# Kernel tuning notes

Hardware: AMD Instinct MI355X
Metric: run time of the kernel (lower is better)

## Reference

```python
import jax, jax.numpy as jnp
import numpy as np

V = 50257       # vocab size (leaves of Huffman tree)
N_DEC = V - 1   # internal decision nodes
D = 1024        # input_size
N_EX = 8192     # number of examples (tokens)
MAX_LEN = 24    # max Huffman path depth


def setup_inputs() -> dict:
    key = jax.random.key(0)
    k_x, k_w, k_t, k_p, k_c, k_l = jax.random.split(key, 6)
    x = jax.random.normal(k_x, (N_EX, D), dtype=jnp.float32)
    W = jax.random.normal(k_w, (N_DEC, D), dtype=jnp.float32) * 0.02
    t = jax.random.randint(k_t, (N_EX,), 0, V, dtype=jnp.int32)
    # padded per-leaf tree paths: decision-node indices and +/-1 branch codes
    paths = jax.random.randint(k_p, (V, MAX_LEN), 0, N_DEC, dtype=jnp.int32)
    codes = jnp.where(jax.random.bernoulli(k_c, 0.5, (V, MAX_LEN)), 1.0, -1.0).astype(jnp.float32)
    lens = jax.random.randint(k_l, (V,), 1, MAX_LEN + 1, dtype=jnp.int32)
    return {"x": x, "W": W, "t": t, "paths": paths, "codes": codes, "lens": lens}


def reference(x, W, t, paths, codes, lens):
    # Per-example tree path: gather the decision nodes / codes for each target leaf.
    node_idx = paths[t]            # [N_EX, MAX_LEN] int32
    code = codes[t]                # [N_EX, MAX_LEN] +/-1
    mask = (jnp.arange(MAX_LEN)[None, :] < lens[t][:, None]).astype(x.dtype)  # [N_EX, MAX_LEN]
    # Irregular gather of W rows along each path, then per-step dot products.
    Wp = W[node_idx]               # [N_EX, MAX_LEN, D]
    wxy = code * jnp.einsum('nd,nld->nl', x, Wp)   # [N_EX, MAX_LEN]
    # Per-decision binary log-loss: log(1 + exp(-wxy)), masked to true path length.
    ls = jax.nn.softplus(-wxy) * mask
    return ls.sum()
```

## Files before the change

### kernel.cpp

```cpp
#include <hip/hip_runtime.h>
#include <math.h>

#define HS_D       1024
#define HS_MAXLEN  24

__global__ __launch_bounds__(256) void hsm_ex_kernel(
    const float* __restrict__ x,
    const float* __restrict__ W,
    const int*   __restrict__ t,
    const int*   __restrict__ paths,
    const float* __restrict__ codes,
    const int*   __restrict__ lens,
    float*       __restrict__ ws,
    int n_ex)
{
    const int tid  = threadIdx.x;
    const int lane = tid & 63;
    const int n = __builtin_amdgcn_readfirstlane(blockIdx.x * 4 + (tid >> 6));
    if (n >= n_ex) return;

    const int leaf = __builtin_amdgcn_readfirstlane(t[n]);
    const int L    = __builtin_amdgcn_readfirstlane(lens[leaf]);

    const float4* x4 = (const float4*)(x + (size_t)n * HS_D);
    float4 xf[4];
#pragma unroll
    for (int j = 0; j < 4; ++j) xf[j] = x4[j * 64 + lane];

    const int*   prow = paths + leaf * HS_MAXLEN;
    const float* crow = codes + leaf * HS_MAXLEN;

    float vsum = 0.0f;

    for (int l0 = 0; l0 < L; l0 += 2) {
        const int  l1 = l0 + 1;
        const bool v1 = (l1 < L);

        const int   node0 = __builtin_amdgcn_readfirstlane(prow[l0]);
        const float c0    = crow[l0];
        const int   node1 = __builtin_amdgcn_readfirstlane(v1 ? prow[l1] : node0);
        const float c1    = v1 ? crow[l1] : 1.0f;

        const float4* w0 = (const float4*)(W + (size_t)node0 * HS_D);
        const float4* w1 = (const float4*)(W + (size_t)node1 * HS_D);

        float4 wf0[4], wf1[4];
#pragma unroll
        for (int j = 0; j < 4; ++j) wf0[j] = w0[j * 64 + lane];
#pragma unroll
        for (int j = 0; j < 4; ++j) wf1[j] = w1[j * 64 + lane];

        float d0 = 0.0f, d1 = 0.0f;
#pragma unroll
        for (int j = 0; j < 4; ++j) {
            d0 += xf[j].x * wf0[j].x + xf[j].y * wf0[j].y
                + xf[j].z * wf0[j].z + xf[j].w * wf0[j].w;
            d1 += xf[j].x * wf1[j].x + xf[j].y * wf1[j].y
                + xf[j].z * wf1[j].z + xf[j].w * wf1[j].w;
        }

#pragma unroll
        for (int off = 32; off > 0; off >>= 1) {
            d0 += __shfl_xor(d0, off);
            d1 += __shfl_xor(d1, off);
        }

        const float z0 = -c0 * d0;
        float v = fmaxf(z0, 0.0f) + log1pf(expf(-fabsf(z0)));
        if (v1) {
            const float z1 = -c1 * d1;
            v += fmaxf(z1, 0.0f) + log1pf(expf(-fabsf(z1)));
        }
        vsum += v;
    }

    if (lane == 0) ws[n] = vsum;
}

__global__ __launch_bounds__(256) void hsm_finish_kernel(
    const float* __restrict__ ws, float* __restrict__ out, int n_ex)
{
    __shared__ float part[4];
    const int tid = threadIdx.x;

    float s = 0.0f;
    const int n4 = n_ex >> 2;
    const float4* w4 = (const float4*)ws;
    for (int k = tid; k < n4; k += 256) {
        const float4 v = w4[k];
        s += v.x + v.y + v.z + v.w;
    }
    if (tid < (n_ex & 3)) s += ws[(n_ex & ~3) + tid];

#pragma unroll
    for (int off = 32; off > 0; off >>= 1)
        s += __shfl_xor(s, off);

    if ((tid & 63) == 0) part[tid >> 6] = s;
    __syncthreads();
    if (tid == 0) out[0] = part[0] + part[1] + part[2] + part[3];
}

extern "C" void kernel_launch(void* const* d_in, const int* in_sizes, int n_in,
                              void* d_out, int out_size, void* d_ws, size_t ws_size,
                              hipStream_t stream) {
    const float* x     = (const float*)d_in[0];
    const float* W     = (const float*)d_in[1];
    const int*   t     = (const int*)  d_in[2];
    const int*   paths = (const int*)  d_in[3];
    const float* codes = (const float*)d_in[4];
    const int*   lens  = (const int*)  d_in[5];
    float* out = (float*)d_out;
    float* ws  = (float*)d_ws;

    const int n_ex = in_sizes[2];

    const int n_blocks = (n_ex + 3) / 4;
    hsm_ex_kernel<<<n_blocks, 256, 0, stream>>>(x, W, t, paths, codes, lens,
                                                ws, n_ex);
    hsm_finish_kernel<<<1, 256, 0, stream>>>(ws, out, n_ex);
}
```

Before: 335.0 us.

## Flatten tree-path pairs into a compacted work list, one wavefront per pair

A new build kernel expands each example's Huffman path into packed 64-bit (node0, node1, example, code-sign) pair entries, compacted through an atomic counter. The pair kernel then gives each wavefront one pair, which removes the serial per-example loop over variable path lengths and exposes more independent memory-latency parallelism. Per-pair losses are accumulated with float atomics into 512 buckets that the finish kernel sums. In exchange it adds a workspace memset, an extra launch, reloads x once per pair (from cache), and launches waves for the maximum pair count, many of which exit immediately.

```diff
diff --git a/kernel.cpp b/kernel.cpp
--- a/kernel.cpp
+++ b/kernel.cpp
@@ -3,99 +3,126 @@
 
 #define HS_D       1024
 #define HS_MAXLEN  24
+#define HS_MAXPAIR 12
+#define HS_NBUCKET 512
 
-__global__ __launch_bounds__(256) void hsm_ex_kernel(
-    const float* __restrict__ x,
-    const float* __restrict__ W,
+#define WS_BUCKET_OFF 64
+#define WS_WL_OFF     4096
+
+
+__global__ __launch_bounds__(64) void hsm_build_kernel(
     const int*   __restrict__ t,
     const int*   __restrict__ paths,
     const float* __restrict__ codes,
     const int*   __restrict__ lens,
-    float*       __restrict__ ws,
+    int*                 counter,
+    unsigned long long* __restrict__ wl,
     int n_ex)
+{
+    const int n = blockIdx.x * 64 + threadIdx.x;
+    if (n >= n_ex) return;
+
+    const int leaf  = t[n];
+    const int L     = lens[leaf];
+    const int npair = (L + 1) >> 1;
+
+    const int4*   p4 = (const int4*)(paths + leaf * HS_MAXLEN);
+    const float4* c4 = (const float4*)(codes + leaf * HS_MAXLEN);
+    int   pa[HS_MAXLEN];
+    float ca[HS_MAXLEN];
+#pragma unroll
+    for (int j = 0; j < HS_MAXLEN / 4; ++j) {
+        const int4   pv = p4[j];
+        const float4 cv = c4[j];
+        pa[4*j+0] = pv.x; pa[4*j+1] = pv.y; pa[4*j+2] = pv.z; pa[4*j+3] = pv.w;
+        ca[4*j+0] = cv.x; ca[4*j+1] = cv.y; ca[4*j+2] = cv.z; ca[4*j+3] = cv.w;
+    }
+
+    const int base = atomicAdd(counter, npair);
+
+#pragma unroll
+    for (int p = 0; p < HS_MAXPAIR; ++p) {
+        if (p < npair) {
+            const int  l0 = 2 * p, l1 = l0 + 1;
+            const bool v1 = (l1 < L);
+            const int  node0 = pa[l0];
+            const int  node1 = v1 ? pa[l1] : node0;
+            const unsigned c0s = (ca[l0] < 0.0f) ? 1u : 0u;
+            const unsigned c1s = (v1 && ca[l1] < 0.0f) ? 1u : 0u;
+            const unsigned lo  = (unsigned)node0 | ((unsigned)node1 << 16);
+            const unsigned hi  = (unsigned)n | (c0s << 24) | (c1s << 25)
+                               | (v1 ? (1u << 26) : 0u) | (1u << 28);
+            wl[base + p] = ((unsigned long long)hi << 32) | lo;
+        }
+    }
+}
+
+__global__ __launch_bounds__(256) void hsm_pair_kernel(
+    const float* __restrict__ x,
+    const float* __restrict__ W,
+    const unsigned long long* __restrict__ wl,
+    float*       __restrict__ buckets)
 {
     const int tid  = threadIdx.x;
     const int lane = tid & 63;
-    const int n = __builtin_amdgcn_readfirstlane(blockIdx.x * 4 + (tid >> 6));
-    if (n >= n_ex) return;
+    const int gw   = blockIdx.x * 4 + (tid >> 6);
 
-    const int leaf = __builtin_amdgcn_readfirstlane(t[n]);
-    const int L    = __builtin_amdgcn_readfirstlane(lens[leaf]);
+    const unsigned long long e = wl[gw];
+    const unsigned hi = (unsigned)(e >> 32);
+    if (!(hi & (1u << 28))) return;
 
-    const float4* x4 = (const float4*)(x + (size_t)n * HS_D);
-    float4 xf[4];
+    const unsigned lo = (unsigned)e;
+    const int n     = __builtin_amdgcn_readfirstlane((int)(hi & 0xFFFFFF));
+    const int node0 = __builtin_amdgcn_readfirstlane((int)(lo & 0xFFFFu));
+    const int node1 = __builtin_amdgcn_readfirstlane((int)(lo >> 16));
+    const float c0  = (hi & (1u << 24)) ? -1.0f : 1.0f;
+    const float c1  = (hi & (1u << 25)) ? -1.0f : 1.0f;
+    const float v1f = (hi & (1u << 26)) ? 1.0f : 0.0f;
+
+    const float4* x4 = (const float4*)(x + (size_t)n     * HS_D);
+    const float4* w0 = (const float4*)(W + (size_t)node0 * HS_D);
+    const float4* w1 = (const float4*)(W + (size_t)node1 * HS_D);
+
+    float4 xf[4], wf0[4], wf1[4];
 #pragma unroll
-    for (int j = 0; j < 4; ++j) xf[j] = x4[j * 64 + lane];
+    for (int j = 0; j < 4; ++j) xf[j]  = x4[j * 64 + lane];
+#pragma unroll
+    for (int j = 0; j < 4; ++j) wf0[j] = w0[j * 64 + lane];
+#pragma unroll
+    for (int j = 0; j < 4; ++j) wf1[j] = w1[j * 64 + lane];
 
-    const int*   prow = paths + leaf * HS_MAXLEN;
-    const float* crow = codes + leaf * HS_MAXLEN;
-
-    float vsum = 0.0f;
-
-    for (int l0 = 0; l0 < L; l0 += 2) {
-        const int  l1 = l0 + 1;
-        const bool v1 = (l1 < L);
-
-        const int   node0 = __builtin_amdgcn_readfirstlane(prow[l0]);
-        const float c0    = crow[l0];
-        const int   node1 = __builtin_amdgcn_readfirstlane(v1 ? prow[l1] : node0);
-        const float c1    = v1 ? crow[l1] : 1.0f;
-
-        const float4* w0 = (const float4*)(W + (size_t)node0 * HS_D);
-        const float4* w1 = (const float4*)(W + (size_t)node1 * HS_D);
-
-        float4 wf0[4], wf1[4];
+    float d0 = 0.0f, d1 = 0.0f;
 #pragma unroll
-        for (int j = 0; j < 4; ++j) wf0[j] = w0[j * 64 + lane];
-#pragma unroll
-        for (int j = 0; j < 4; ++j) wf1[j] = w1[j * 64 + lane];
-
-        float d0 = 0.0f, d1 = 0.0f;
-#pragma unroll
-        for (int j = 0; j < 4; ++j) {
-            d0 += xf[j].x * wf0[j].x + xf[j].y * wf0[j].y
-                + xf[j].z * wf0[j].z + xf[j].w * wf0[j].w;
-            d1 += xf[j].x * wf1[j].x + xf[j].y * wf1[j].y
-                + xf[j].z * wf1[j].z + xf[j].w * wf1[j].w;
-        }
+    for (int j = 0; j < 4; ++j) {
+        d0 += xf[j].x * wf0[j].x + xf[j].y * wf0[j].y
+            + xf[j].z * wf0[j].z + xf[j].w * wf0[j].w;
+        d1 += xf[j].x * wf1[j].x + xf[j].y * wf1[j].y
+            + xf[j].z * wf1[j].z + xf[j].w * wf1[j].w;
+    }
 
 #pragma unroll
-        for (int off = 32; off > 0; off >>= 1) {
-            d0 += __shfl_xor(d0, off);
-            d1 += __shfl_xor(d1, off);
-        }
-
-        const float z0 = -c0 * d0;
-        float v = fmaxf(z0, 0.0f) + log1pf(expf(-fabsf(z0)));
-        if (v1) {
-            const float z1 = -c1 * d1;
-            v += fmaxf(z1, 0.0f) + log1pf(expf(-fabsf(z1)));
-        }
-        vsum += v;
+    for (int off = 32; off > 0; off >>= 1) {
+        d0 += __shfl_xor(d0, off);
+        d1 += __shfl_xor(d1, off);
     }
 
-    if (lane == 0) ws[n] = vsum;
+    const float z0 = -c0 * d0;
+    float v = fmaxf(z0, 0.0f) + log1pf(expf(-fabsf(z0)));
+    const float z1 = -c1 * d1;
+    v += v1f * (fmaxf(z1, 0.0f) + log1pf(expf(-fabsf(z1))));
+
+    if (lane == 0) atomicAdd(&buckets[gw & (HS_NBUCKET - 1)], v);
 }
 
 __global__ __launch_bounds__(256) void hsm_finish_kernel(
-    const float* __restrict__ ws, float* __restrict__ out, int n_ex)
+    const float* __restrict__ buckets, float* __restrict__ out)
 {
     __shared__ float part[4];
     const int tid = threadIdx.x;
-
-    float s = 0.0f;
-    const int n4 = n_ex >> 2;
-    const float4* w4 = (const float4*)ws;
-    for (int k = tid; k < n4; k += 256) {
-        const float4 v = w4[k];
-        s += v.x + v.y + v.z + v.w;
-    }
-    if (tid < (n_ex & 3)) s += ws[(n_ex & ~3) + tid];
-
+    float s = buckets[tid] + buckets[tid + 256];
 #pragma unroll
     for (int off = 32; off > 0; off >>= 1)
         s += __shfl_xor(s, off);
-
     if ((tid & 63) == 0) part[tid >> 6] = s;
     __syncthreads();
     if (tid == 0) out[0] = part[0] + part[1] + part[2] + part[3];
@@ -111,12 +138,20 @@
     const float* codes = (const float*)d_in[4];
     const int*   lens  = (const int*)  d_in[5];
     float* out = (float*)d_out;
-    float* ws  = (float*)d_ws;
 
-    const int n_ex = in_sizes[2];
+    int*                counter = (int*)d_ws;
+    float*              buckets = (float*)((char*)d_ws + WS_BUCKET_OFF);
+    unsigned long long* wl      = (unsigned long long*)((char*)d_ws + WS_WL_OFF);
 
-    const int n_blocks = (n_ex + 3) / 4;
-    hsm_ex_kernel<<<n_blocks, 256, 0, stream>>>(x, W, t, paths, codes, lens,
-                                                ws, n_ex);
-    hsm_finish_kernel<<<1, 256, 0, stream>>>(ws, out, n_ex);
+    const int n_ex      = in_sizes[2];
+    const int max_pairs = n_ex * HS_MAXPAIR;
+
+    hipMemsetAsync(d_ws, 0, WS_WL_OFF + (size_t)(max_pairs + 4) * 8, stream);
+
+    hsm_build_kernel<<<(n_ex + 63) / 64, 64, 0, stream>>>(
+        t, paths, codes, lens, counter, wl, n_ex);
+
+    const int n_blocks = (max_pairs + 3) / 4;
+    hsm_pair_kernel<<<n_blocks, 256, 0, stream>>>(x, W, wl, buckets);
+    hsm_finish_kernel<<<1, 256, 0, stream>>>(buckets, out);
 }
```

Result: faster. 328.4 us (-2.0%).

## Restructure path loop into separate load, reduce and loss phases

Applied to the files above, without the earlier changes.

Turns the per-pair path loop into fully unrolled phases. Node indices are prefetched first, then every W-row dot product is issued, then all cross-lane shuffle reductions run, then the softplus terms are summed. Pulling the shuffle reductions out of the load loop lets the W loads for later pairs go out without waiting on each pair's reduction, which exposes more memory-level parallelism. The cost is more registers (24 partial sums plus the index arrays) and possibly lower occupancy. Unrolling with runtime guards may also give heavier control flow.

```diff
diff --git a/kernel.cpp b/kernel.cpp
--- a/kernel.cpp
+++ b/kernel.cpp
@@ -3,6 +3,7 @@
 
 #define HS_D       1024
 #define HS_MAXLEN  24
+#define HS_MAXPAIR 12
 
 __global__ __launch_bounds__(256) void hsm_ex_kernel(
     const float* __restrict__ x,
@@ -16,11 +17,12 @@
 {
     const int tid  = threadIdx.x;
     const int lane = tid & 63;
-    const int n = __builtin_amdgcn_readfirstlane(blockIdx.x * 4 + (tid >> 6));
+    const int n    = blockIdx.x * 4 + (tid >> 6);
     if (n >= n_ex) return;
 
-    const int leaf = __builtin_amdgcn_readfirstlane(t[n]);
-    const int L    = __builtin_amdgcn_readfirstlane(lens[leaf]);
+    const int leaf  = __builtin_amdgcn_readfirstlane(t[n]);
+    const int L     = __builtin_amdgcn_readfirstlane(lens[leaf]);
+    const int npair = (L + 1) >> 1;
 
     const float4* x4 = (const float4*)(x + (size_t)n * HS_D);
     float4 xf[4];
@@ -30,48 +32,68 @@
     const int*   prow = paths + leaf * HS_MAXLEN;
     const float* crow = codes + leaf * HS_MAXLEN;
 
-    float vsum = 0.0f;
+    int nd0[HS_MAXPAIR], nd1[HS_MAXPAIR];
+#pragma unroll
+    for (int p = 0; p < HS_MAXPAIR; ++p) {
+        if (p < npair) {
+            const int  l0 = 2 * p, l1 = l0 + 1;
+            const bool v1 = (l1 < L);
+            nd0[p] = __builtin_amdgcn_readfirstlane(prow[l0]);
+            nd1[p] = __builtin_amdgcn_readfirstlane(v1 ? prow[l1] : prow[l0]);
+        }
+    }
 
-    for (int l0 = 0; l0 < L; l0 += 2) {
-        const int  l1 = l0 + 1;
-        const bool v1 = (l1 < L);
-
-        const int   node0 = __builtin_amdgcn_readfirstlane(prow[l0]);
-        const float c0    = crow[l0];
-        const int   node1 = __builtin_amdgcn_readfirstlane(v1 ? prow[l1] : node0);
-        const float c1    = v1 ? crow[l1] : 1.0f;
-
-        const float4* w0 = (const float4*)(W + (size_t)node0 * HS_D);
-        const float4* w1 = (const float4*)(W + (size_t)node1 * HS_D);
-
-        float4 wf0[4], wf1[4];
+    float d[2 * HS_MAXPAIR];
 #pragma unroll
-        for (int j = 0; j < 4; ++j) wf0[j] = w0[j * 64 + lane];
-#pragma unroll
-        for (int j = 0; j < 4; ++j) wf1[j] = w1[j * 64 + lane];
-
-        float d0 = 0.0f, d1 = 0.0f;
-#pragma unroll
-        for (int j = 0; j < 4; ++j) {
-            d0 += xf[j].x * wf0[j].x + xf[j].y * wf0[j].y
-                + xf[j].z * wf0[j].z + xf[j].w * wf0[j].w;
-            d1 += xf[j].x * wf1[j].x + xf[j].y * wf1[j].y
-                + xf[j].z * wf1[j].z + xf[j].w * wf1[j].w;
-        }
+    for (int k = 0; k < 2 * HS_MAXPAIR; ++k) d[k] = 0.0f;
 
 #pragma unroll
-        for (int off = 32; off > 0; off >>= 1) {
-            d0 += __shfl_xor(d0, off);
-            d1 += __shfl_xor(d1, off);
+    for (int p = 0; p < HS_MAXPAIR; ++p) {
+        if (p < npair) {
+            const float4* w0 = (const float4*)(W + (size_t)nd0[p] * HS_D);
+            const float4* w1 = (const float4*)(W + (size_t)nd1[p] * HS_D);
+            float4 wf0[4], wf1[4];
+#pragma unroll
+            for (int j = 0; j < 4; ++j) wf0[j] = w0[j * 64 + lane];
+#pragma unroll
+            for (int j = 0; j < 4; ++j) wf1[j] = w1[j * 64 + lane];
+
+            float s0 = 0.0f, s1 = 0.0f;
+#pragma unroll
+            for (int j = 0; j < 4; ++j) {
+                s0 += xf[j].x * wf0[j].x + xf[j].y * wf0[j].y
+                    + xf[j].z * wf0[j].z + xf[j].w * wf0[j].w;
+                s1 += xf[j].x * wf1[j].x + xf[j].y * wf1[j].y
+                    + xf[j].z * wf1[j].z + xf[j].w * wf1[j].w;
+            }
+            d[2 * p]     = s0;
+            d[2 * p + 1] = s1;
         }
+    }
 
-        const float z0 = -c0 * d0;
-        float v = fmaxf(z0, 0.0f) + log1pf(expf(-fabsf(z0)));
-        if (v1) {
-            const float z1 = -c1 * d1;
-            v += fmaxf(z1, 0.0f) + log1pf(expf(-fabsf(z1)));
+#pragma unroll
+    for (int p = 0; p < HS_MAXPAIR; ++p) {
+        if (p < npair) {
+#pragma unroll
+            for (int off = 32; off > 0; off >>= 1) {
+                d[2 * p]     += __shfl_xor(d[2 * p],     off);
+                d[2 * p + 1] += __shfl_xor(d[2 * p + 1], off);
+            }
         }
-        vsum += v;
+    }
+
+    float vsum = 0.0f;
+#pragma unroll
+    for (int p = 0; p < HS_MAXPAIR; ++p) {
+        if (p < npair) {
+            const int l0 = 2 * p, l1 = l0 + 1;
+            const float z0 = -crow[l0] * d[2 * p];
+            vsum += fmaxf(z0, 0.0f) + log1pf(expf(-fabsf(z0)));
+            if (l1 < L) {
+                const float z1 = -crow[l1] * d[2 * p + 1];
+                vsum += fmaxf(z1, 0.0f) + log1pf(expf(-fabsf(z1)));
+            }
+        }
     }
 
     if (lane == 0) ws[n] = vsum;
```

New measurement: 410.6 us. 22.6% more time.
